# Kernel optimization log

Measured on AMD Instinct MI355X. Metric: run time of the kernel, lower is better.

## Reference

```python
import jax, jax.numpy as jnp
import numpy as np

B, S, HID = 2, 2048, 2048
H, DN, DR, KVR, DV = 16, 128, 64, 512, 128
THETA = 10000.0
EPS = 1e-6
SCALE = (DN + DR) ** -0.5  # softmax_scale = q_head_dim ** -0.5 (rope_scaling is None)


def setup_inputs() -> dict:
    key = jax.random.key(0)
    ks = jax.random.split(key, 8)
    std = 0.02
    return {
        "hidden_states": jax.random.normal(ks[0], (B, S, HID), jnp.float32),
        "q_nope_weight": jax.random.normal(ks[1], (H * DN, HID), jnp.float32) * std,
        "q_pe_weight": jax.random.normal(ks[2], (H * DR, HID), jnp.float32) * std,
        "kv_a_weight": jax.random.normal(ks[3], (KVR + DR, HID), jnp.float32) * std,
        "kv_a_ln_weight": jnp.ones((KVR,), jnp.float32),
        "k_b_weight": jax.random.normal(ks[4], (H, DN, KVR), jnp.float32) * std,
        "v_b_weight": jax.random.normal(ks[5], (H, DV, KVR), jnp.float32) * std,
        "o_weight": jax.random.normal(ks[6], (HID, H * DV), jnp.float32) * std,
        "position_ids": jnp.arange(S, dtype=jnp.int32)[None, :],
    }


def _rotate_half(x):
    x1, x2 = jnp.split(x, 2, axis=-1)
    return jnp.concatenate((-x2, x1), axis=-1)


def _interleave(x):
    # torch: x.view(..., d//2, 2).transpose(-1, -2).reshape(..., d)
    *lead, d = x.shape
    x = x.reshape(*lead, d // 2, 2)
    x = jnp.swapaxes(x, -1, -2)
    return x.reshape(*lead, d)


def reference(hidden_states, q_nope_weight, q_pe_weight, kv_a_weight,
              kv_a_ln_weight, k_b_weight, v_b_weight, o_weight, position_ids):
    b, s, _ = hidden_states.shape
    # Q projections, split into no-rope and rope parts per head
    q_nope = jnp.einsum('bsh,ndh->bnsd', hidden_states, q_nope_weight.reshape(H, DN, HID))
    q_pe = jnp.einsum('bsh,ndh->bnsd', hidden_states, q_pe_weight.reshape(H, DR, HID))
    # Joint low-rank KV + shared rope-key projection (MQA-style)
    ckv_kpe = jnp.einsum('bsh,ch->bsc', hidden_states, kv_a_weight)  # [b,s,KVR+DR]
    ckv, k_pe = ckv_kpe[..., :KVR], ckv_kpe[..., KVR:]
    # RMSNorm over the compressed latent (kv_a_layernorm)
    var = jnp.mean(jnp.square(ckv), axis=-1, keepdims=True)
    ckv = ckv * jax.lax.rsqrt(var + EPS) * kv_a_ln_weight  # [b,s,KVR]
    # Rotary tables: cos/sin indexed by position_ids, broadcast over heads
    inv_freq = 1.0 / (THETA ** (jnp.arange(0, DR, 2, dtype=jnp.float32) / DR))
    t = position_ids.astype(jnp.float32)                 # [1,s]
    freqs = t[..., None] * inv_freq                      # [1,s,DR/2]
    emb = jnp.concatenate((freqs, freqs), axis=-1)       # [1,s,DR]
    cos = jnp.cos(emb)[:, None]                          # [1,1,s,DR]
    sin = jnp.sin(emb)[:, None]
    # Partial RoPE with the interleave permutation from apply_rotary_pos_emb
    q_pe = _interleave(q_pe)
    k_pe = _interleave(k_pe[:, None])                    # [b,1,s,DR]
    q_pe = q_pe * cos + _rotate_half(q_pe) * sin
    k_pe = (k_pe * cos + _rotate_half(k_pe) * sin)[:, 0] # [b,s,DR]
    # Weight absorption: fold k_b into q, attend directly in the latent space
    q_lat = jnp.einsum('bnsd,ndc->bnsc', q_nope, k_b_weight)  # [b,H,s,KVR]
    scores = (jnp.einsum('bnsc,btc->bnst', q_lat, ckv)
              + jnp.einsum('bnsd,btd->bnst', q_pe, k_pe)) * SCALE
    mask = jnp.tril(jnp.ones((s, s), dtype=bool))
    scores = jnp.where(mask, scores, jnp.finfo(scores.dtype).min)
    attn = jax.nn.softmax(scores, axis=-1)
    # Attention output in the latent space, then expand with v_b and o_proj
    out_lat = jnp.einsum('bnst,btc->bnsc', attn, ckv)         # [b,H,s,KVR]
    v_out = jnp.einsum('bnsc,ndc->bnsd', out_lat, v_b_weight) # [b,H,s,DV]
    v_out = v_out.transpose(0, 2, 1, 3).reshape(b, s, H * DV)
    return jnp.einsum('bsf,hf->bsh', v_out, o_weight)
```

## Files before the change

### kernel.cpp

```cpp
#include <hip/hip_runtime.h>
#include <hip/hip_bf16.h>


typedef __hip_bfloat16 bf16;
typedef __bf16 v8bf __attribute__((ext_vector_type(8)));
typedef float  v4f  __attribute__((ext_vector_type(4)));
typedef unsigned int v4u __attribute__((ext_vector_type(4)));

#define S_    2048
#define SCALE_F 0.07216878364870322f

__device__ __forceinline__ void st1(float* p, float v){ *p = v; }
__device__ __forceinline__ void st1(bf16* p, float v){ *p = __float2bfloat16(v); }
__device__ __forceinline__ unsigned short bfb(float x){
  return __builtin_bit_cast(unsigned short, __float2bfloat16(x));
}
__device__ __forceinline__ unsigned pk2(float a, float b){
  return (unsigned)bfb(a) | ((unsigned)bfb(b) << 16);
}

typedef const void __attribute__((address_space(1)))* gas_t;
typedef void __attribute__((address_space(3)))* las_t;
__device__ __forceinline__ void g2l16(const void* g, void* l){
  __builtin_amdgcn_global_load_lds((gas_t)g, (las_t)l, 16, 0, 0);
}

__global__ void cossin_kernel(const int* __restrict__ pos, float* __restrict__ cosT,
                              float* __restrict__ sinT){
  int idx = blockIdx.x*256 + threadIdx.x;
  int i = idx & 31, s = idx >> 5;
  float t = (float)pos[s];
  float freq = t * powf(10000.0f, -(float)i/32.0f);
  cosT[idx] = cosf(freq);
  sinT[idx] = sinf(freq);
}

__global__ void castf2b_kernel(const float* __restrict__ src, bf16* __restrict__ dst, int n8){
  int i = blockIdx.x*256 + threadIdx.x;
  if (i >= n8) return;
  const float4* s = (const float4*)src;
  float4 a = s[2*i], b = s[2*i+1];
  uint4 o; o.x = pk2(a.x,a.y); o.y = pk2(a.z,a.w); o.z = pk2(b.x,b.y); o.w = pk2(b.z,b.w);
  ((uint4*)dst)[i] = o;
}

__global__ void cast4_kernel(const float* __restrict__ a, bf16* __restrict__ da,
                             const float* __restrict__ b, bf16* __restrict__ db,
                             const float* __restrict__ c, bf16* __restrict__ dc,
                             const float* __restrict__ d, bf16* __restrict__ dd){
  int j = blockIdx.x*256 + threadIdx.x;
  const float* s; bf16* t;
  if (j < 1048576){ s=a; t=da; }
  else if ((j-=1048576) < 524288){ s=b; t=db; }
  else if ((j-=524288) < 262144){ s=c; t=dc; }
  else if ((j-=262144) < 147456){ s=d; t=dd; }
  else return;
  float4 x = ((const float4*)s)[2*j], y = ((const float4*)s)[2*j+1];
  uint4 o; o.x=pk2(x.x,x.y); o.y=pk2(x.z,x.w); o.z=pk2(y.x,y.y); o.w=pk2(y.z,y.w);
  ((uint4*)t)[j] = o;
}

template<typename TC>
__global__ __launch_bounds__(256) void gemm2_kernel(
    const bf16* __restrict__ A, int lda, int aDiv, long aS1, long aS2,
    const bf16* __restrict__ W, int ldw, int wDiv, long wS1, long wS2,
    TC* __restrict__ C, int ldc, int cDiv, long cS1, long cS2,
    int N, int K, float alpha)
{
  int z = blockIdx.z;
  A += (long)(z/aDiv)*aS1 + (long)(z%aDiv)*aS2;
  W += (long)(z/wDiv)*wS1 + (long)(z%wDiv)*wS2;
  C += (long)(z/cDiv)*cS1 + (long)(z%cDiv)*cS2;
  __shared__ bf16 As[2][4096];
  __shared__ bf16 Ws[2][4096];
  const int tid = threadIdx.x;
  const int w = tid>>6, l = tid&63, g = l>>4, c16 = l&15;
  const int wr = (w>>1)*64, wc = (w&1)*64;
  const int row0 = blockIdx.y*128, col0 = blockIdx.x*128;

  const long aO1 = (long)(row0 + (tid>>2))*lda + (tid&3)*8;
  const long aO2 = (long)(row0 + 64 + (tid>>2))*lda + (tid&3)*8;
  int wr1 = col0 + (tid>>2);      if (wr1 > N-1) wr1 = N-1;
  int wr2 = col0 + 64 + (tid>>2); if (wr2 > N-1) wr2 = N-1;
  const long wO1 = (long)wr1*ldw + (tid&3)*8;
  const long wO2 = (long)wr2*ldw + (tid&3)*8;

  v4f acc[4][4];
  #pragma unroll
  for (int i=0;i<4;i++)
    #pragma unroll
    for (int j=0;j<4;j++) acc[i][j] = (v4f){0.f,0.f,0.f,0.f};

  auto STAGE = [&](int k0, int bsel){
    g2l16(A + aO1 + k0, &As[bsel][tid*8]);
    g2l16(A + aO2 + k0, &As[bsel][2048 + tid*8]);
    g2l16(W + wO1 + k0, &Ws[bsel][tid*8]);
    g2l16(W + wO2 + k0, &Ws[bsel][2048 + tid*8]);
  };
  STAGE(0, 0);
  __syncthreads();
  const int nk = K >> 5;
  for (int t=0; t<nk; ++t){
    const int cur = t & 1;
    if (t+1 < nk) STAGE((t+1)*32, cur^1);
    v8bf af[4], bw[4];
    #pragma unroll
    for (int mi=0;mi<4;mi++) af[mi] = *(const v8bf*)&As[cur][(wr+mi*16+c16)*32 + g*8];
    #pragma unroll
    for (int ni=0;ni<4;ni++) bw[ni] = *(const v8bf*)&Ws[cur][(wc+ni*16+c16)*32 + g*8];
    #pragma unroll
    for (int mi=0;mi<4;mi++)
      #pragma unroll
      for (int ni=0;ni<4;ni++)
        acc[mi][ni] = __builtin_amdgcn_mfma_f32_16x16x32_bf16(af[mi], bw[ni], acc[mi][ni], 0,0,0);
    __syncthreads();
  }
  #pragma unroll
  for (int mi=0;mi<4;mi++)
    #pragma unroll
    for (int ni=0;ni<4;ni++)
      #pragma unroll
      for (int r=0;r<4;r++){
        int row = row0 + wr + mi*16 + g*4 + r;
        int col = col0 + wc + ni*16 + c16;
        if (col < N) st1(C + (long)row*ldc + col, acc[mi][ni][r]*alpha);
      }
}

__global__ __launch_bounds__(256) void proj3_kernel(
    const bf16* __restrict__ A,
    const bf16* __restrict__ Wq, const bf16* __restrict__ Wp, const bf16* __restrict__ Wc,
    bf16* __restrict__ Cq, bf16* __restrict__ Cp, bf16* __restrict__ Cc)
{
  const int bx = blockIdx.x;
  const bf16* W; bf16* C; int ldc, N, col0;
  if (bx < 16){ W = Wq; C = Cq; ldc = 2048; N = 2048; col0 = bx*128; }
  else if (bx < 24){ W = Wp; C = Cp; ldc = 1024; N = 1024; col0 = (bx-16)*128; }
  else { W = Wc; C = Cc; ldc = 576; N = 576; col0 = (bx-24)*128; }
  __shared__ bf16 As[2][4096];
  __shared__ bf16 Ws[2][4096];
  const int tid = threadIdx.x;
  const int w = tid>>6, l = tid&63, g = l>>4, c16 = l&15;
  const int wr = (w>>1)*64, wc = (w&1)*64;
  const int row0 = blockIdx.y*128;

  const long aO1 = (long)(row0 + (tid>>2))*2048 + (tid&3)*8;
  const long aO2 = (long)(row0 + 64 + (tid>>2))*2048 + (tid&3)*8;
  int wr1 = col0 + (tid>>2);      if (wr1 > N-1) wr1 = N-1;
  int wr2 = col0 + 64 + (tid>>2); if (wr2 > N-1) wr2 = N-1;
  const long wO1 = (long)wr1*2048 + (tid&3)*8;
  const long wO2 = (long)wr2*2048 + (tid&3)*8;

  v4f acc[4][4];
  #pragma unroll
  for (int i=0;i<4;i++)
    #pragma unroll
    for (int j=0;j<4;j++) acc[i][j] = (v4f){0.f,0.f,0.f,0.f};

  auto STAGE = [&](int k0, int bsel){
    g2l16(A + aO1 + k0, &As[bsel][tid*8]);
    g2l16(A + aO2 + k0, &As[bsel][2048 + tid*8]);
    g2l16(W + wO1 + k0, &Ws[bsel][tid*8]);
    g2l16(W + wO2 + k0, &Ws[bsel][2048 + tid*8]);
  };
  STAGE(0, 0);
  __syncthreads();
  for (int t=0; t<64; ++t){
    const int cur = t & 1;
    if (t+1 < 64) STAGE((t+1)*32, cur^1);
    v8bf af[4], bw[4];
    #pragma unroll
    for (int mi=0;mi<4;mi++) af[mi] = *(const v8bf*)&As[cur][(wr+mi*16+c16)*32 + g*8];
    #pragma unroll
    for (int ni=0;ni<4;ni++) bw[ni] = *(const v8bf*)&Ws[cur][(wc+ni*16+c16)*32 + g*8];
    #pragma unroll
    for (int mi=0;mi<4;mi++)
      #pragma unroll
      for (int ni=0;ni<4;ni++)
        acc[mi][ni] = __builtin_amdgcn_mfma_f32_16x16x32_bf16(af[mi], bw[ni], acc[mi][ni], 0,0,0);
    __syncthreads();
  }
  #pragma unroll
  for (int mi=0;mi<4;mi++)
    #pragma unroll
    for (int ni=0;ni<4;ni++)
      #pragma unroll
      for (int r=0;r<4;r++){
        int row = row0 + wr + mi*16 + g*4 + r;
        int col = col0 + wc + ni*16 + c16;
        if (col < N) C[(long)row*ldc + col] = __float2bfloat16(acc[mi][ni][r]);
      }
}

__global__ __launch_bounds__(256) void kbT_kernel(const float* __restrict__ kb,
                                                  bf16* __restrict__ kbT){
  __shared__ bf16 t[64][65];
  int h = blockIdx.z, c0 = blockIdx.x*64, d0 = blockIdx.y*64;
  const float* src = kb + ((long)h*128 + d0)*512 + c0;
  #pragma unroll
  for (int i=0;i<16;i++){
    int idx = i*256 + threadIdx.x;
    int dl = idx>>6, cl = idx&63;
    t[dl][cl] = __float2bfloat16(src[(long)dl*512 + cl]);
  }
  __syncthreads();
  bf16* dst = kbT + ((long)h*512 + c0)*128 + d0;
  #pragma unroll
  for (int i=0;i<16;i++){
    int idx = i*256 + threadIdx.x;
    int cl = idx>>6, dl = idx&63;
    dst[(long)cl*128 + dl] = t[dl][cl];
  }
}

__global__ __launch_bounds__(256) void tposeV_kernel(const bf16* __restrict__ Kb,
                                                     bf16* __restrict__ Kd){
  __shared__ bf16 t[64][65];
  int b = blockIdx.z, s0 = blockIdx.y*64, d0 = blockIdx.x*64;
  const bf16* src = Kb + ((long)(b*S_ + s0))*576 + d0;
  #pragma unroll
  for (int i=0;i<16;i++){
    int idx = i*256 + threadIdx.x;
    int sl = idx>>6, dl = idx&63;
    t[sl][dl] = src[(long)sl*576 + dl];
  }
  __syncthreads();
  bf16* dst = Kd + ((long)(b*512 + d0))*S_ + s0;
  #pragma unroll
  for (int i=0;i<16;i++){
    int idx = i*256 + threadIdx.x;
    int dl = idx>>6, sl = idx&63;
    dst[(long)dl*S_ + sl] = t[sl][dl];
  }
}

__global__ __launch_bounds__(256) void build_k_kernel(
    const bf16* __restrict__ ckv_kpe, const float* __restrict__ ln_w,
    const float* __restrict__ cosT, const float* __restrict__ sinT,
    bf16* __restrict__ Kb)
{
  int row = blockIdx.x;
  int s = row & (S_-1);
  int tid = threadIdx.x;
  const bf16* src = ckv_kpe + (long)row*576;
  float x0 = __bfloat162float(src[tid*2]), x1 = __bfloat162float(src[tid*2+1]);
  float ss = x0*x0 + x1*x1;
  #pragma unroll
  for (int o=32;o>=1;o>>=1) ss += __shfl_xor(ss, o, 64);
  __shared__ float wss[4];
  int wid = tid>>6, lane = tid&63;
  if (lane==0) wss[wid] = ss;
  __syncthreads();
  float tot = wss[0]+wss[1]+wss[2]+wss[3];
  float rs = rsqrtf(tot*(1.0f/512.0f) + 1e-6f);
  bf16* dst = Kb + (long)row*576;
  dst[tid*2]   = __float2bfloat16(x0*rs*ln_w[tid*2]);
  dst[tid*2+1] = __float2bfloat16(x1*rs*ln_w[tid*2+1]);
  if (tid < 32) {
    float p0 = __bfloat162float(src[512 + tid*2]);
    float p1 = __bfloat162float(src[512 + tid*2 + 1]);
    float c = cosT[s*32+tid], sn = sinT[s*32+tid];
    dst[512+tid] = __float2bfloat16(p0*c - p1*sn);
    dst[544+tid] = __float2bfloat16(p1*c + p0*sn);
  }
}

__global__ void rope_q_kernel(const bf16* __restrict__ qpe,
                              const float* __restrict__ cosT, const float* __restrict__ sinT,
                              bf16* __restrict__ Qb)
{
  int idx = blockIdx.x*256 + threadIdx.x;
  int i = idx & 31;
  int s = (idx >> 5) & (S_-1);
  int z = idx >> 16;
  int b = z >> 4, n = z & 15;
  long base = ((long)(b*S_+s))*1024 + n*64 + 2*i;
  float x0 = __bfloat162float(qpe[base]), x1 = __bfloat162float(qpe[base+1]);
  float c = cosT[s*32+i], sn = sinT[s*32+i];
  bf16* dst = Qb + ((long)z*S_ + s)*576;
  dst[512+i] = __float2bfloat16((x0*c - x1*sn)*SCALE_F);
  dst[544+i] = __float2bfloat16((x1*c + x0*sn)*SCALE_F);
}

#define K0_OFF 0
#define K1_OFF 36864
#define V0_OFF 73728
#define V1_OFF 106496
#define SX_OFF 139264
#define SMEM_BYTES 155648

__global__ __launch_bounds__(512, 2) void attn_mfma_kernel(
    const bf16* __restrict__ Qg, const bf16* __restrict__ Kg,
    const bf16* __restrict__ Vdg, bf16* __restrict__ Og)
{
  extern __shared__ char smem[];
  const int tid = threadIdx.x;
  const int w   = tid >> 6;
  const int l   = tid & 63;
  const int g   = l >> 4;
  const int c16 = l & 15;
  const int rg  = w & 3;
  const int dh  = w >> 2;
  const int R   = rg * 16;
  const int Dh  = dh * 256;
  const int DQb = dh * 576;
  char* SXw = smem + SX_OFF + rg*4096 + dh*2048;
  char* SXr = smem + SX_OFF + rg*4096 + (1-dh)*2048;

  const int lin = blockIdx.x;
  const int k8 = lin & 7;
  const int b  = k8 >> 2;
  const int u  = (lin >> 3)*4 + (k8 & 3);
  const int n  = u & 15;
  const int pr = u >> 4;
  const int z  = b*16 + n;

  const char* kb0 = (const char*)Kg  + (long)b*S_*1152;
  const char* vd0 = (const char*)Vdg + (long)b*512*S_*2;

  int kOffG[5], kOffL[5], vOffG[4], vOffL[4];
  #pragma unroll
  for (int it=0; it<4; it++){
    int c = it*512 + tid;
    int kcol = c/72, j = c - kcol*72;
    kOffG[it] = kcol*1152 + ((j ^ (kcol&7))<<4);
    kOffL[it] = c*16;
  }
  {
    int c = 2048 + tid;
    int kcol = c/72, j = c - kcol*72;
    kOffG[4] = kcol*1152 + ((j ^ (kcol&7))<<4);
    kOffL[4] = c*16;
  }
  #pragma unroll
  for (int it=0; it<4; it++){
    int c = it*512 + tid;
    int s = c>>3, uu = (c&7) ^ (s&7);
    int d = 2*s + (uu>>2), j = uu&3;
    vOffG[it] = d*(S_*2) + j*16;
    vOffL[it] = c*16;
  }

  auto STAGE = [&](int tt, char* kd, char* vd){
    const char* ksrc = kb0 + (long)tt*36864;
    #pragma unroll
    for (int it=0; it<4; it++) g2l16(ksrc + kOffG[it], kd + kOffL[it]);
    if (tid < 256) g2l16(ksrc + kOffG[4], kd + kOffL[4]);
    const char* vsrc = vd0 + (long)tt*64;
    #pragma unroll
    for (int it=0; it<4; it++) g2l16(vsrc + vOffG[it], vd + vOffL[it]);
  };

  const int kRow0 = c16*1152;
  const int kRow1 = kRow0 + 16*1152;
  int kSlot[9];
  #pragma unroll
  for (int kk=0;kk<9;kk++)
    kSlot[kk] = (((dh*36 + kk*4 + g) ^ (c16&7))<<4);
  int vRd[16];
  #pragma unroll
  for (int cb=0;cb<16;cb++){
    int d = Dh + cb*16 + c16;
    int vu = ((((d&1)<<2)) | g) ^ ((d>>1)&7);
    vRd[cb] = (d>>1)*128 + (vu<<4);
  }
  const int sxf0 = c16*128 + (((2*g + 0 + c16)&7)<<4);
  const int sxf1 = c16*128 + (((2*g + 1 + c16)&7)<<4);
  const int srcA = ((2*g)&3)*16 + c16;
  const int srcB = ((2*g+1)&3)*16 + c16;
  const bool hiG = (g >= 2);
  const int shflBase = l & 48;

  for (int ph = 0; ph < 2; ++ph){
    const int qt = ph ? (31 - pr) : pr;
    const int q0 = qt * 64;

    v8bf qf[9];
    {
      const char* qgb = (const char*)Qg + ((long)z*S_ + q0 + R + c16)*1152 + DQb;
      #pragma unroll
      for (int kk=0;kk<9;kk++) qf[kk] = *(const v8bf*)(qgb + kk*64 + g*16);
    }
    v4f acc[16];
    #pragma unroll
    for (int i=0;i<16;i++) acc[i] = (v4f){0.f,0.f,0.f,0.f};
    float mL = -1e30f;
    float lsumL = 0.f;

    const int ntile = 2*qt + 2;
    __syncthreads();
    STAGE(0, smem + K0_OFF, smem + V0_OFF);

    for (int t = 0; t < ntile; ++t){
      asm volatile("s_waitcnt vmcnt(0)" ::: "memory");
      __syncthreads();
      char* kB = smem + ((t&1) ? K1_OFF : K0_OFF);
      char* vB = smem + ((t&1) ? V1_OFF : V0_OFF);
      if (t+1 < ntile)
        STAGE(t+1, smem + (((t+1)&1) ? K1_OFF : K0_OFF),
                    smem + (((t+1)&1) ? V1_OFF : V0_OFF));

      v4f s0 = (v4f){0.f,0.f,0.f,0.f}, s1 = (v4f){0.f,0.f,0.f,0.f};
      #pragma unroll
      for (int kk=0;kk<9;kk++){
        v8bf kf0 = *(const v8bf*)(kB + kRow0 + kSlot[kk]);
        v8bf kf1 = *(const v8bf*)(kB + kRow1 + kSlot[kk]);
        s0 = __builtin_amdgcn_mfma_f32_16x16x32_bf16(kf0, qf[kk], s0, 0,0,0);
        s1 = __builtin_amdgcn_mfma_f32_16x16x32_bf16(kf1, qf[kk], s1, 0,0,0);
      }
      *(float4*)(SXw + sxf0) = make_float4(s0[0], s0[1], s1[0], s1[1]);
      *(float4*)(SXw + sxf1) = make_float4(s0[2], s0[3], s1[2], s1[3]);
      asm volatile("s_waitcnt lgkmcnt(0)" ::: "memory");
      __builtin_amdgcn_s_barrier();
      __builtin_amdgcn_sched_barrier(0);
      {
        float4 o0 = *(const float4*)(SXr + sxf0);
        float4 o1 = *(const float4*)(SXr + sxf1);
        s0[0] += o0.x; s0[1] += o0.y; s1[0] += o0.z; s1[1] += o0.w;
        s0[2] += o1.x; s0[3] += o1.y; s1[2] += o1.z; s1[3] += o1.w;
      }
      if (t >= ntile-2){
        int kt0 = t*32;
        int qrow = q0 + R + c16;
        #pragma unroll
        for (int r=0;r<4;r++){
          if (kt0 + g*4 + r > qrow)      s0[r] = -1e30f;
          if (kt0 + 16 + g*4 + r > qrow) s1[r] = -1e30f;
        }
      }
      float pm = fmaxf(fmaxf(fmaxf(s0[0],s0[1]),fmaxf(s0[2],s0[3])),
                       fmaxf(fmaxf(s1[0],s1[1]),fmaxf(s1[2],s1[3])));
      pm = fmaxf(pm, __shfl_xor(pm, 16));
      pm = fmaxf(pm, __shfl_xor(pm, 32));
      float alv = 1.0f;
      if (pm > mL + 8.0f){ alv = __expf(mL - pm); mL = pm; }
      float p0[4], p1[4];
      float sv = 0.f;
      #pragma unroll
      for (int r=0;r<4;r++){
        p0[r] = __expf(s0[r] - mL);
        p1[r] = __expf(s1[r] - mL);
        sv += p0[r] + p1[r];
      }
      sv += __shfl_xor(sv, 16);
      sv += __shfl_xor(sv, 32);
      lsumL = lsumL*alv + sv;
      unsigned u0 = pk2(p0[0],p0[1]), u1 = pk2(p0[2],p0[3]);
      unsigned u2 = pk2(p1[0],p1[1]), u3 = pk2(p1[2],p1[3]);
      unsigned a0 = __shfl(u0, srcA), a1 = __shfl(u1, srcA);
      unsigned a2 = __shfl(u2, srcA), a3 = __shfl(u3, srcA);
      unsigned b0 = __shfl(u0, srcB), b1 = __shfl(u1, srcB);
      unsigned b2 = __shfl(u2, srcB), b3 = __shfl(u3, srcB);
      v4u paw;
      paw.x = hiG ? a2 : a0;  paw.y = hiG ? a3 : a1;
      paw.z = hiG ? b2 : b0;  paw.w = hiG ? b3 : b1;
      v8bf pa = __builtin_bit_cast(v8bf, paw);
      if (!__all((int)(alv == 1.0f))){
        float alr[4];
        #pragma unroll
        for (int r=0;r<4;r++) alr[r] = __shfl(alv, shflBase | (g*4+r));
        #pragma unroll
        for (int cb=0;cb<16;cb++)
          #pragma unroll
          for (int r=0;r<4;r++) acc[cb][r] *= alr[r];
      }
      #pragma unroll
      for (int cb=0;cb<16;cb++){
        v8bf vf = *(const v8bf*)(vB + vRd[cb]);
        acc[cb] = __builtin_amdgcn_mfma_f32_16x16x32_bf16(pa, vf, acc[cb], 0,0,0);
      }
    }
    float invL = 1.0f / lsumL;
    float invr[4];
    #pragma unroll
    for (int r=0;r<4;r++) invr[r] = __shfl(invL, shflBase | (g*4+r));
    #pragma unroll
    for (int cb=0;cb<16;cb++)
      #pragma unroll
      for (int r=0;r<4;r++){
        int qrow = q0 + R + g*4 + r;
        Og[((long)z*S_ + qrow)*512 + Dh + cb*16 + c16] = __float2bfloat16(acc[cb][r]*invr[r]);
      }
  }
}

extern "C" void kernel_launch(void* const* d_in, const int* in_sizes, int n_in,
                              void* d_out, int out_size, void* d_ws, size_t ws_size,
                              hipStream_t stream)
{
  const float* hidden = (const float*)d_in[0];
  const float* qn_w   = (const float*)d_in[1];
  const float* qpe_w  = (const float*)d_in[2];
  const float* kva_w  = (const float*)d_in[3];
  const float* ln_w   = (const float*)d_in[4];
  const float* kb_w   = (const float*)d_in[5];
  const float* vb_w   = (const float*)d_in[6];
  const float* o_w    = (const float*)d_in[7];
  const int*   pos    = (const int*)d_in[8];
  float* out = (float*)d_out;
  char* ws = (char*)d_ws;

  float* cosT  = (float*)(ws);
  float* sinT  = (float*)(ws + 262144);
  bf16*  ckvb  = (bf16*) (ws + 524288);
  bf16*  vbb   = (bf16*) (ws + 524288);
  bf16*  Qb    = (bf16*) (ws + 5242880);
  bf16*  ob    = (bf16*) (ws + 5242880);
  bf16*  Kb    = (bf16*) (ws + 80740352);
  bf16*  outl  = (bf16*) (ws + 85458944);
  bf16*  qnopeb= (bf16*) (ws + 85458944);
  bf16*  qpeb  = (bf16*) (ws + 102236160);
  bf16*  kbT   = (bf16*) (ws + 110624768);
  bf16*  hb    = (bf16*) (ws + 112721920);
  bf16*  qnb   = (bf16*) (ws + 129499136);
  bf16*  qpw   = (bf16*) (ws + 137887744);
  bf16*  kvab  = (bf16*) (ws + 142082048);
  bf16*  voutb = (bf16*) (ws + 152567808);
  bf16*  Kd    = (bf16*) (ws + 169345024);

  static_assert(sizeof(v8bf) == 16, "v8bf must be 16B");
  hipFuncSetAttribute((const void*)attn_mfma_kernel,
                      hipFuncAttributeMaxDynamicSharedMemorySize, SMEM_BYTES);

  cossin_kernel<<<256, 256, 0, stream>>>(pos, cosT, sinT);

  cast4_kernel<<<7744, 256, 0, stream>>>(hidden, hb, qn_w, qnb, qpe_w, qpw, kva_w, kvab);

  proj3_kernel<<<dim3(29,32,1),256,0,stream>>>(hb, qnb, qpw, kvab,
                                               qnopeb, qpeb, ckvb);

  kbT_kernel<<<dim3(8,2,16), 256, 0, stream>>>(kb_w, kbT);
  build_k_kernel<<<4096, 256, 0, stream>>>(ckvb, ln_w, cosT, sinT, Kb);
  castf2b_kernel<<<512, 256, 0, stream>>>(vb_w, vbb, 131072);
  tposeV_kernel<<<dim3(8,32,2), 256, 0, stream>>>(Kb, Kd);
  rope_q_kernel<<<8192, 256, 0, stream>>>(qpeb, cosT, sinT, Qb);

  gemm2_kernel<bf16><<<dim3(4,16,32),256,0,stream>>>(
      qnopeb,2048, 16,(long)S_*2048,128,  kbT,128, 16,0,65536,
      Qb,576, 1,(long)S_*576,0,  512,128, SCALE_F);

  attn_mfma_kernel<<<dim3(512), 512, SMEM_BYTES, stream>>>(Qb, Kb, Kd, outl);

  castf2b_kernel<<<2048, 256, 0, stream>>>(o_w, ob, 524288);

  gemm2_kernel<bf16><<<dim3(1,16,32),256,0,stream>>>(
      outl,512, 1,(long)S_*512,0,  vbb,512, 16,0,65536,
      voutb,2048, 16,(long)S_*2048,128,  128,512, 1.f);

  gemm2_kernel<float><<<dim3(16,32,1),256,0,stream>>>(
      voutb,2048, 1,0,0,  ob,2048, 1,0,0,  out,2048, 1,0,0,  2048,2048, 1.f);
}
```

Measured before the change: 540.2 us.

## Shrink attention key tile to 16 and drop double buffering for higher occupancy

The attention kernel now processes 16 keys per iteration instead of 32 and uses a single LDS buffer instead of double buffering. This cuts shared memory from about 152KB to 44KB and raises the launch bounds to 4 blocks per CU. The PV product switches to the 16x16x16 bf16 MFMA, which uses the P fragment directly and removes the lane shuffles. In exchange there are twice as many loop iterations and barriers, and global loads are no longer overlapped with compute inside a block, so it relies on other resident blocks to hide latency.

```diff
diff --git a/kernel.cpp b/kernel.cpp
--- a/kernel.cpp
+++ b/kernel.cpp
@@ -6,6 +6,7 @@
 typedef __bf16 v8bf __attribute__((ext_vector_type(8)));
 typedef float  v4f  __attribute__((ext_vector_type(4)));
 typedef unsigned int v4u __attribute__((ext_vector_type(4)));
+typedef unsigned int v2u __attribute__((ext_vector_type(2)));
 
 #define S_    2048
 #define SCALE_F 0.07216878364870322f
@@ -17,6 +18,10 @@
 }
 __device__ __forceinline__ unsigned pk2(float a, float b){
   return (unsigned)bfb(a) | ((unsigned)bfb(b) << 16);
+}
+__device__ __forceinline__ v4f mfma16(v2u a, v2u b, v4f c){
+  asm("v_mfma_f32_16x16x16_bf16 %0, %1, %2, %0" : "+v"(c) : "v"(a), "v"(b));
+  return c;
 }
 
 typedef const void __attribute__((address_space(1)))* gas_t;
@@ -282,18 +287,18 @@
   dst[544+i] = __float2bfloat16((x1*c + x0*sn)*SCALE_F);
 }
 
-#define K0_OFF 0
-#define K1_OFF 36864
-#define V0_OFF 73728
-#define V1_OFF 106496
-#define SX_OFF 139264
-#define SMEM_BYTES 155648
-
-__global__ __launch_bounds__(512, 2) void attn_mfma_kernel(
+#define K_OFF  0
+#define V_OFF  18432
+#define SX_OFF 34816
+#define SMEM_BYTES 45056
+
+__global__ __launch_bounds__(512, 4) void attn_mfma_kernel(
     const bf16* __restrict__ Qg, const bf16* __restrict__ Kg,
     const bf16* __restrict__ Vdg, bf16* __restrict__ Og)
 {
   extern __shared__ char smem[];
+  char* kB = smem + K_OFF;
+  char* vB = smem + V_OFF;
   const int tid = threadIdx.x;
   const int w   = tid >> 6;
   const int l   = tid & 63;
@@ -304,8 +309,8 @@
   const int R   = rg * 16;
   const int Dh  = dh * 256;
   const int DQb = dh * 576;
-  char* SXw = smem + SX_OFF + rg*4096 + dh*2048;
-  char* SXr = smem + SX_OFF + rg*4096 + (1-dh)*2048;
+  char* SXw = smem + SX_OFF + rg*2560 + dh*1280;
+  char* SXr = smem + SX_OFF + rg*2560 + (1-dh)*1280;
 
   const int lin = blockIdx.x;
   const int k8 = lin & 7;
@@ -318,41 +323,42 @@
   const char* kb0 = (const char*)Kg  + (long)b*S_*1152;
   const char* vd0 = (const char*)Vdg + (long)b*512*S_*2;
 
-  int kOffG[5], kOffL[5], vOffG[4], vOffL[4];
-  #pragma unroll
-  for (int it=0; it<4; it++){
+  int kOffG[3], kOffL[3];
+  #pragma unroll
+  for (int it=0; it<2; it++){
     int c = it*512 + tid;
     int kcol = c/72, j = c - kcol*72;
     kOffG[it] = kcol*1152 + ((j ^ (kcol&7))<<4);
     kOffL[it] = c*16;
   }
   {
-    int c = 2048 + tid;
+    int c = 1024 + tid;
     int kcol = c/72, j = c - kcol*72;
-    kOffG[4] = kcol*1152 + ((j ^ (kcol&7))<<4);
-    kOffL[4] = c*16;
-  }
-  #pragma unroll
-  for (int it=0; it<4; it++){
-    int c = it*512 + tid;
-    int s = c>>3, uu = (c&7) ^ (s&7);
-    int d = 2*s + (uu>>2), j = uu&3;
-    vOffG[it] = d*(S_*2) + j*16;
-    vOffL[it] = c*16;
-  }
-
-  auto STAGE = [&](int tt, char* kd, char* vd){
-    const char* ksrc = kb0 + (long)tt*36864;
-    #pragma unroll
-    for (int it=0; it<4; it++) g2l16(ksrc + kOffG[it], kd + kOffL[it]);
-    if (tid < 256) g2l16(ksrc + kOffG[4], kd + kOffL[4]);
-    const char* vsrc = vd0 + (long)tt*64;
-    #pragma unroll
-    for (int it=0; it<4; it++) g2l16(vsrc + vOffG[it], vd + vOffL[it]);
+    kOffG[2] = kcol*1152 + ((j ^ (kcol&7))<<4);
+    kOffL[2] = c*16;
+  }
+  int vOffG[2], vOffL[2];
+  #pragma unroll
+  for (int it=0; it<2; it++){
+    int s = it*512 + tid;
+    int key = (s>>4)&7;
+    int v = s ^ key;
+    int d = v>>1, h = v&1;
+    vOffG[it] = d*4096 + h*16;
+    vOffL[it] = s*16;
+  }
+
+  auto STAGE = [&](int tt){
+    const char* ksrc = kb0 + (long)tt*18432;
+    g2l16(ksrc + kOffG[0], kB + kOffL[0]);
+    g2l16(ksrc + kOffG[1], kB + kOffL[1]);
+    if (tid < 128) g2l16(ksrc + kOffG[2], kB + kOffL[2]);
+    const char* vsrc = vd0 + (long)tt*32;
+    g2l16(vsrc + vOffG[0], vB + vOffL[0]);
+    g2l16(vsrc + vOffG[1], vB + vOffL[1]);
   };
 
   const int kRow0 = c16*1152;
-  const int kRow1 = kRow0 + 16*1152;
   int kSlot[9];
   #pragma unroll
   for (int kk=0;kk<9;kk++)
@@ -361,19 +367,16 @@
   #pragma unroll
   for (int cb=0;cb<16;cb++){
     int d = Dh + cb*16 + c16;
-    int vu = ((((d&1)<<2)) | g) ^ ((d>>1)&7);
-    vRd[cb] = (d>>1)*128 + (vu<<4);
-  }
-  const int sxf0 = c16*128 + (((2*g + 0 + c16)&7)<<4);
-  const int sxf1 = c16*128 + (((2*g + 1 + c16)&7)<<4);
-  const int srcA = ((2*g)&3)*16 + c16;
-  const int srcB = ((2*g+1)&3)*16 + c16;
-  const bool hiG = (g >= 2);
+    int slot = ((d<<1)|(g>>1)) ^ ((d>>3)&7);
+    vRd[cb] = slot*16 + (g&1)*8;
+  }
+  const int sxo = c16*80 + ((g ^ (c16&3))<<4);
   const int shflBase = l & 48;
 
   for (int ph = 0; ph < 2; ++ph){
     const int qt = ph ? (31 - pr) : pr;
     const int q0 = qt * 64;
+    const int ntile = 4*qt + 4;
 
     v8bf qf[9];
     {
@@ -387,74 +390,49 @@
     float mL = -1e30f;
     float lsumL = 0.f;
 
-    const int ntile = 2*qt + 2;
-    __syncthreads();
-    STAGE(0, smem + K0_OFF, smem + V0_OFF);
-
     for (int t = 0; t < ntile; ++t){
+      __syncthreads();
+      STAGE(t);
       asm volatile("s_waitcnt vmcnt(0)" ::: "memory");
       __syncthreads();
-      char* kB = smem + ((t&1) ? K1_OFF : K0_OFF);
-      char* vB = smem + ((t&1) ? V1_OFF : V0_OFF);
-      if (t+1 < ntile)
-        STAGE(t+1, smem + (((t+1)&1) ? K1_OFF : K0_OFF),
-                    smem + (((t+1)&1) ? V1_OFF : V0_OFF));
-
-      v4f s0 = (v4f){0.f,0.f,0.f,0.f}, s1 = (v4f){0.f,0.f,0.f,0.f};
+
+      v4f s0 = (v4f){0.f,0.f,0.f,0.f};
       #pragma unroll
       for (int kk=0;kk<9;kk++){
-        v8bf kf0 = *(const v8bf*)(kB + kRow0 + kSlot[kk]);
-        v8bf kf1 = *(const v8bf*)(kB + kRow1 + kSlot[kk]);
-        s0 = __builtin_amdgcn_mfma_f32_16x16x32_bf16(kf0, qf[kk], s0, 0,0,0);
-        s1 = __builtin_amdgcn_mfma_f32_16x16x32_bf16(kf1, qf[kk], s1, 0,0,0);
-      }
-      *(float4*)(SXw + sxf0) = make_float4(s0[0], s0[1], s1[0], s1[1]);
-      *(float4*)(SXw + sxf1) = make_float4(s0[2], s0[3], s1[2], s1[3]);
+        v8bf kf = *(const v8bf*)(kB + kRow0 + kSlot[kk]);
+        s0 = __builtin_amdgcn_mfma_f32_16x16x32_bf16(kf, qf[kk], s0, 0,0,0);
+      }
+      *(float4*)(SXw + sxo) = make_float4(s0[0], s0[1], s0[2], s0[3]);
       asm volatile("s_waitcnt lgkmcnt(0)" ::: "memory");
       __builtin_amdgcn_s_barrier();
       __builtin_amdgcn_sched_barrier(0);
       {
-        float4 o0 = *(const float4*)(SXr + sxf0);
-        float4 o1 = *(const float4*)(SXr + sxf1);
-        s0[0] += o0.x; s0[1] += o0.y; s1[0] += o0.z; s1[1] += o0.w;
-        s0[2] += o1.x; s0[3] += o1.y; s1[2] += o1.z; s1[3] += o1.w;
-      }
-      if (t >= ntile-2){
-        int kt0 = t*32;
+        float4 o = *(const float4*)(SXr + sxo);
+        s0[0] += o.x; s0[1] += o.y; s0[2] += o.z; s0[3] += o.w;
+      }
+      if (t >= ntile-4){
+        int kt0 = t*16;
         int qrow = q0 + R + c16;
         #pragma unroll
-        for (int r=0;r<4;r++){
-          if (kt0 + g*4 + r > qrow)      s0[r] = -1e30f;
-          if (kt0 + 16 + g*4 + r > qrow) s1[r] = -1e30f;
-        }
-      }
-      float pm = fmaxf(fmaxf(fmaxf(s0[0],s0[1]),fmaxf(s0[2],s0[3])),
-                       fmaxf(fmaxf(s1[0],s1[1]),fmaxf(s1[2],s1[3])));
+        for (int r=0;r<4;r++)
+          if (kt0 + g*4 + r > qrow) s0[r] = -1e30f;
+      }
+      float pm = fmaxf(fmaxf(s0[0],s0[1]), fmaxf(s0[2],s0[3]));
       pm = fmaxf(pm, __shfl_xor(pm, 16));
       pm = fmaxf(pm, __shfl_xor(pm, 32));
       float alv = 1.0f;
       if (pm > mL + 8.0f){ alv = __expf(mL - pm); mL = pm; }
-      float p0[4], p1[4];
-      float sv = 0.f;
-      #pragma unroll
-      for (int r=0;r<4;r++){
-        p0[r] = __expf(s0[r] - mL);
-        p1[r] = __expf(s1[r] - mL);
-        sv += p0[r] + p1[r];
-      }
+      float p0 = __expf(s0[0] - mL);
+      float p1 = __expf(s0[1] - mL);
+      float p2 = __expf(s0[2] - mL);
+      float p3 = __expf(s0[3] - mL);
+      float sv = (p0+p1) + (p2+p3);
       sv += __shfl_xor(sv, 16);
       sv += __shfl_xor(sv, 32);
       lsumL = lsumL*alv + sv;
-      unsigned u0 = pk2(p0[0],p0[1]), u1 = pk2(p0[2],p0[3]);
-      unsigned u2 = pk2(p1[0],p1[1]), u3 = pk2(p1[2],p1[3]);
-      unsigned a0 = __shfl(u0, srcA), a1 = __shfl(u1, srcA);
-      unsigned a2 = __shfl(u2, srcA), a3 = __shfl(u3, srcA);
-      unsigned b0 = __shfl(u0, srcB), b1 = __shfl(u1, srcB);
-      unsigned b2 = __shfl(u2, srcB), b3 = __shfl(u3, srcB);
-      v4u paw;
-      paw.x = hiG ? a2 : a0;  paw.y = hiG ? a3 : a1;
-      paw.z = hiG ? b2 : b0;  paw.w = hiG ? b3 : b1;
-      v8bf pa = __builtin_bit_cast(v8bf, paw);
+      v2u pa;
+      pa.x = pk2(p0, p1);
+      pa.y = pk2(p2, p3);
       if (!__all((int)(alv == 1.0f))){
         float alr[4];
         #pragma unroll
@@ -466,8 +444,8 @@
       }
       #pragma unroll
       for (int cb=0;cb<16;cb++){
-        v8bf vf = *(const v8bf*)(vB + vRd[cb]);
-        acc[cb] = __builtin_amdgcn_mfma_f32_16x16x32_bf16(pa, vf, acc[cb], 0,0,0);
+        v2u vf = *(const v2u*)(vB + vRd[cb]);
+        acc[cb] = mfma16(pa, vf, acc[cb]);
       }
     }
     float invL = 1.0f / lsumL;
```

After: 1.524 ms. 182% more time.
